# Optimization experiments

Hardware: AMD Instinct MI355X
Metric: run time of the kernel (lower is better)

Reference implementation:

```python
import jax, jax.numpy as jnp
import numpy as np


def setup_inputs() -> dict:
    key = jax.random.key(0)
    ks = jax.random.split(key, 9)
    B = 1024
    s = 0.05
    return {
        "x": jax.random.normal(ks[0], (B, 1024), dtype=jnp.float32),
        "u1": jax.random.normal(ks[1], (8, 8, 16), dtype=jnp.float32) * s,
        "u2": jax.random.normal(ks[2], (8, 8, 16), dtype=jnp.float32) * s,
        "u3": jax.random.normal(ks[3], (16, 16, 16), dtype=jnp.float32) * s,
        "b2": jax.random.normal(ks[4], (16, 16, 16), dtype=jnp.float32) * s,
        "b1_core": jax.random.normal(ks[5], (16, 16), dtype=jnp.float32) * s,
        "bias1": jax.random.normal(ks[6], (8, 8, 16), dtype=jnp.float32) * s,
        "fc2_w": jax.random.normal(ks[7], (10, 1024), dtype=jnp.float32) * s,
        "fc2_b": jax.random.normal(ks[8], (10,), dtype=jnp.float32) * s,
    }


def reference(x, u1, u2, u3, b2, b1_core, bias1, fc2_w, fc2_b):
    batch = x.shape[0]
    t = x.reshape(batch, 8, 8, 16)                       # z a b c
    t = jnp.einsum('zabc,ade->zbcde', t, u1)             # (z,8,16,8,16)
    t = jnp.einsum('zabcd,def->zabcef', t, b2)           # (z,8,16,8,16,16)
    t = jnp.einsum('zabcde,afd->zbcef', t, u2)           # (z,16,8,16,8)
    t = jnp.einsum('zabcd,ce->zabde', t, b1_core)        # (z,16,8,8,16)
    t = jnp.einsum('zabcd,aed->zbce', t, u3)             # (z,8,8,16)
    t = t + bias1
    h = jax.nn.relu(t.reshape(batch, 1024))
    return h @ fc2_w.T + fc2_b
```

## Files before the change

### kernel.cpp

```cpp
#include <hip/hip_runtime.h>


using s16x8 = __attribute__((ext_vector_type(8))) short;
using f32x4 = __attribute__((ext_vector_type(4))) float;

__device__ inline short f2bf(float f) {
    unsigned u = __builtin_bit_cast(unsigned, f);
    u += 0x7fffu + ((u >> 16) & 1u);
    return (short)(u >> 16);
}

__global__ __launch_bounds__(256) void k_prep(
    const float* __restrict__ x, const float* __restrict__ u1,
    const float* __restrict__ u2, const float* __restrict__ u3,
    const float* __restrict__ b2, const float* __restrict__ b1c,
    short* __restrict__ Wb, short* __restrict__ Xb) {
    const int blk = blockIdx.x;
    const int tid = threadIdx.x;

    if (blk >= 256) {
        const int base = (blk - 256) * 4096 + tid * 16;
#pragma unroll
        for (int h = 0; h < 2; ++h) {
            float4 f0 = *(const float4*)&x[base + h * 8];
            float4 f1 = *(const float4*)&x[base + h * 8 + 4];
            s16x8 v;
            v[0] = f2bf(f0.x); v[1] = f2bf(f0.y);
            v[2] = f2bf(f0.z); v[3] = f2bf(f0.w);
            v[4] = f2bf(f1.x); v[5] = f2bf(f1.y);
            v[6] = f2bf(f1.z); v[7] = f2bf(f1.w);
            *(s16x8*)&Xb[base + h * 8] = v;
        }
        return;
    }

    __shared__ float b1s[256];
    __shared__ float u1s[128];
    __shared__ float u2s[64 * 17];
    __shared__ float u3s[4096];
    __shared__ float C2t[256 * 17];
    __shared__ float T1s[2048];
    __shared__ float T2s[64 * 17];
    const int d = blk >> 5;
    const int r = (blk >> 2) & 7;
    const int t0 = (blk & 3) * 4;

    b1s[tid] = b1c[tid];
    {
        float4* dst = (float4*)u3s;
        const float4* src = (const float4*)u3;
#pragma unroll
        for (int q = 0; q < 4; ++q) dst[tid + 256 * q] = src[tid + 256 * q];
    }
    if (tid < 64) {
        const float4* src = (const float4*)&u2[tid * 16];
#pragma unroll
        for (int q = 0; q < 4; ++q) {
            float4 v = src[q];
            u2s[tid * 17 + q * 4 + 0] = v.x;
            u2s[tid * 17 + q * 4 + 1] = v.y;
            u2s[tid * 17 + q * 4 + 2] = v.z;
            u2s[tid * 17 + q * 4 + 3] = v.w;
        }
    }
    if (tid < 8) {
#pragma unroll
        for (int e = 0; e < 16; ++e)
            u1s[tid * 16 + e] = u1[(tid * 8 + d) * 16 + e];
    }
    float b2r[16];
    {
        const float4* src = (const float4*)&b2[tid * 16];
#pragma unroll
        for (int q = 0; q < 4; ++q) {
            float4 v = src[q];
            b2r[q * 4 + 0] = v.x; b2r[q * 4 + 1] = v.y;
            b2r[q * 4 + 2] = v.z; b2r[q * 4 + 3] = v.w;
        }
    }
    __syncthreads();

    {
        float accs[16] = {};
#pragma unroll
        for (int q = 0; q < 16; ++q) {
            const float bq = b2r[q];
#pragma unroll
            for (int s = 0; s < 16; ++s) accs[s] += bq * b1s[q * 16 + s];
        }
#pragma unroll
        for (int s = 0; s < 16; ++s) C2t[tid * 17 + s] = accs[s];
    }
    __syncthreads();

    {
        const int p = tid >> 4, s = tid & 15;
#pragma unroll
        for (int a = 0; a < 8; ++a) {
            float acc = 0.f;
#pragma unroll
            for (int e = 0; e < 16; ++e)
                acc += u1s[a * 16 + e] * C2t[(e * 16 + p) * 17 + s];
            T1s[a * 256 + tid] = acc;
        }
    }
    __syncthreads();

#pragma unroll
    for (int j = 0; j < 4; ++j) {
        int idx = tid + 256 * j;
        int ab = idx >> 4, s = idx & 15;
        int a = ab >> 3, b = ab & 7;
        float acc = 0.f;
#pragma unroll
        for (int p = 0; p < 16; ++p)
            acc += T1s[a * 256 + p * 16 + s] * u2s[(b * 8 + r) * 17 + p];
        T2s[ab * 17 + s] = acc;
    }
    __syncthreads();

    {
        const int j = tid >> 6;
        const int t = t0 + j;
        const int col0 = (tid & 63) * 16;
        const int ab = col0 >> 4;
        const float* t2p = &T2s[ab * 17];
        short* wrow = &Wb[(blk * 4 + j) * 1024 + col0];
        s16x8 v0, v1;
#pragma unroll
        for (int c = 0; c < 16; ++c) {
            const float* u3p = &u3s[c * 256 + t * 16];
            float acc = 0.f;
#pragma unroll
            for (int s = 0; s < 16; ++s) acc += t2p[s] * u3p[s];
            short bf = f2bf(acc);
            if (c < 8) v0[c] = bf; else v1[c - 8] = bf;
        }
        *(s16x8*)(wrow) = v0;
        *(s16x8*)(wrow + 8) = v1;
    }
}

#define LDK 136

__global__ __launch_bounds__(256) void k_gemm(
    const short* __restrict__ Xb, const short* __restrict__ Wb,
    float* __restrict__ PH) {
    __shared__ short As[64][LDK];
    __shared__ short Bs[64][LDK];
    const int tid = threadIdx.x;
    const int lane = tid & 63;
    const int w = tid >> 6, wr = w >> 1, wc = w & 1;
    const int o0 = blockIdx.x * 64, z0 = blockIdx.y * 64, kz = blockIdx.z;
    const int srow = tid >> 2;
    const int sc = (tid & 3) * 16;

    const short* xp = &Xb[(z0 + srow) * 1024 + kz * 256 + sc];
    const short* wp = &Wb[(o0 + srow) * 1024 + kz * 256 + sc];

    f32x4 acc[2][2] = {};
    s16x8 ax[4], bx[4];

#pragma unroll
    for (int h = 0; h < 2; ++h)
#pragma unroll
        for (int q = 0; q < 2; ++q) {
            ax[h * 2 + q] = *(const s16x8*)(xp + h * 64 + q * 8);
            bx[h * 2 + q] = *(const s16x8*)(wp + h * 64 + q * 8);
        }

#pragma unroll
    for (int it = 0; it < 2; ++it) {
#pragma unroll
        for (int h = 0; h < 2; ++h)
#pragma unroll
            for (int q = 0; q < 2; ++q) {
                *(s16x8*)&As[srow][sc + h * 64 + q * 8] = ax[h * 2 + q];
                *(s16x8*)&Bs[srow][sc + h * 64 + q * 8] = bx[h * 2 + q];
            }
        __syncthreads();
        if (it == 0) {
#pragma unroll
            for (int h = 0; h < 2; ++h)
#pragma unroll
                for (int q = 0; q < 2; ++q) {
                    ax[h * 2 + q] = *(const s16x8*)(xp + 128 + h * 64 + q * 8);
                    bx[h * 2 + q] = *(const s16x8*)(wp + 128 + h * 64 + q * 8);
                }
        }
#pragma unroll
        for (int ks = 0; ks < 4; ++ks) {
            const int kb = ks * 32 + (lane >> 4) * 8;
            s16x8 a0 = *(const s16x8*)&As[wr * 32 + (lane & 15)][kb];
            s16x8 a1 = *(const s16x8*)&As[wr * 32 + 16 + (lane & 15)][kb];
            s16x8 b0 = *(const s16x8*)&Bs[wc * 32 + (lane & 15)][kb];
            s16x8 b1 = *(const s16x8*)&Bs[wc * 32 + 16 + (lane & 15)][kb];
            acc[0][0] = __builtin_amdgcn_mfma_f32_16x16x32_bf16(a0, b0, acc[0][0], 0, 0, 0);
            acc[0][1] = __builtin_amdgcn_mfma_f32_16x16x32_bf16(a0, b1, acc[0][1], 0, 0, 0);
            acc[1][0] = __builtin_amdgcn_mfma_f32_16x16x32_bf16(a1, b0, acc[1][0], 0, 0, 0);
            acc[1][1] = __builtin_amdgcn_mfma_f32_16x16x32_bf16(a1, b1, acc[1][1], 0, 0, 0);
        }
        __syncthreads();
    }

    float* ph = &PH[(unsigned)kz * 1048576u];
#pragma unroll
    for (int m = 0; m < 2; ++m)
#pragma unroll
        for (int n = 0; n < 2; ++n) {
            const int row = z0 + wr * 32 + m * 16 + (lane >> 4) * 4;
            const int col = o0 + wc * 32 + n * 16 + (lane & 15);
#pragma unroll
            for (int j = 0; j < 4; ++j)
                ph[(row + j) * 1024 + col] = acc[m][n][j];
        }
}

__global__ __launch_bounds__(256) void k_out(
    const float* __restrict__ PH, const float* __restrict__ bias1,
    const float* __restrict__ W2, const float* __restrict__ fc2b,
    float* __restrict__ out) {
    __shared__ float W2s[10][1024];
    const int tid = threadIdx.x;
#pragma unroll
    for (int i = 0; i < 10; ++i) {
        const int idx = tid + 256 * i;
        ((float4*)W2s)[idx] = ((const float4*)W2)[idx];
    }
    __syncthreads();

    const int wid = tid >> 6, lane = tid & 63;
    const int z = blockIdx.x * 4 + wid;
    float part[10];
#pragma unroll
    for (int j = 0; j < 10; ++j) part[j] = 0.f;
#pragma unroll
    for (int i = 0; i < 16; ++i) {
        const int col = lane + 64 * i;
        float h = PH[z * 1024 + col] + PH[1048576 + z * 1024 + col]
                + PH[2097152 + z * 1024 + col] + PH[3145728 + z * 1024 + col];
        h = fmaxf(h + bias1[col], 0.f);
#pragma unroll
        for (int j = 0; j < 10; ++j) part[j] += h * W2s[j][col];
    }
#pragma unroll
    for (int j = 0; j < 10; ++j) {
#pragma unroll
        for (int off = 32; off > 0; off >>= 1) part[j] += __shfl_xor(part[j], off);
    }
    if (lane == 0) {
#pragma unroll
        for (int j = 0; j < 10; ++j) out[z * 10 + j] = part[j] + fc2b[j];
    }
}

extern "C" void kernel_launch(void* const* d_in, const int* in_sizes, int n_in,
                              void* d_out, int out_size, void* d_ws, size_t ws_size,
                              hipStream_t stream) {
    const float* x     = (const float*)d_in[0];
    const float* u1    = (const float*)d_in[1];
    const float* u2    = (const float*)d_in[2];
    const float* u3    = (const float*)d_in[3];
    const float* b2    = (const float*)d_in[4];
    const float* b1c   = (const float*)d_in[5];
    const float* bias1 = (const float*)d_in[6];
    const float* fc2w  = (const float*)d_in[7];
    const float* fc2b  = (const float*)d_in[8];
    float* out = (float*)d_out;

    short* Wb = (short*)d_ws;
    short* Xb = (short*)((char*)d_ws + 2u * 1024u * 1024u);
    float* PH = (float*)((char*)d_ws + 4u * 1024u * 1024u);

    k_prep<<<512, 256, 0, stream>>>(x, u1, u2, u3, b2, b1c, Wb, Xb);
    k_gemm<<<dim3(16, 16, 4), 256, 0, stream>>>(Xb, Wb, PH);
    k_out<<<256, 256, 0, stream>>>(PH, bias1, fc2w, fc2b, out);
}
```

Baseline: 29.03 us.

## Drop LDS staging in GEMM and load MFMA fragments directly from global

The split-K GEMM no longer stages A and B tiles in shared memory with barriers. Each of 8 waves loads its bf16 MFMA fragments straight from global memory and computes a 16x32 output slice over the full 256-long K chunk. This removes LDS writes, reads and syncs and doubles the waves per block. In exchange, A and B data is fetched redundantly across waves and relies on cache hits.

Result: slower. 44.17 us (+52.1%).

```diff
diff --git a/kernel.cpp b/kernel.cpp
--- a/kernel.cpp
+++ b/kernel.cpp
@@ -141,79 +141,41 @@
     }
 }
 
-#define LDK 136
-
-__global__ __launch_bounds__(256) void k_gemm(
+__global__ __launch_bounds__(512) void k_gemm(
     const short* __restrict__ Xb, const short* __restrict__ Wb,
     float* __restrict__ PH) {
-    __shared__ short As[64][LDK];
-    __shared__ short Bs[64][LDK];
     const int tid = threadIdx.x;
     const int lane = tid & 63;
-    const int w = tid >> 6, wr = w >> 1, wc = w & 1;
+    const int wid = tid >> 6;
+    const int band = wid >> 1;
+    const int half = wid & 1;
     const int o0 = blockIdx.x * 64, z0 = blockIdx.y * 64, kz = blockIdx.z;
-    const int srow = tid >> 2;
-    const int sc = (tid & 3) * 16;
-
-    const short* xp = &Xb[(z0 + srow) * 1024 + kz * 256 + sc];
-    const short* wp = &Wb[(o0 + srow) * 1024 + kz * 256 + sc];
-
-    f32x4 acc[2][2] = {};
-    s16x8 ax[4], bx[4];
-
-#pragma unroll
-    for (int h = 0; h < 2; ++h)
-#pragma unroll
-        for (int q = 0; q < 2; ++q) {
-            ax[h * 2 + q] = *(const s16x8*)(xp + h * 64 + q * 8);
-            bx[h * 2 + q] = *(const s16x8*)(wp + h * 64 + q * 8);
-        }
-
-#pragma unroll
-    for (int it = 0; it < 2; ++it) {
-#pragma unroll
-        for (int h = 0; h < 2; ++h)
-#pragma unroll
-            for (int q = 0; q < 2; ++q) {
-                *(s16x8*)&As[srow][sc + h * 64 + q * 8] = ax[h * 2 + q];
-                *(s16x8*)&Bs[srow][sc + h * 64 + q * 8] = bx[h * 2 + q];
-            }
-        __syncthreads();
-        if (it == 0) {
-#pragma unroll
-            for (int h = 0; h < 2; ++h)
-#pragma unroll
-                for (int q = 0; q < 2; ++q) {
-                    ax[h * 2 + q] = *(const s16x8*)(xp + 128 + h * 64 + q * 8);
-                    bx[h * 2 + q] = *(const s16x8*)(wp + 128 + h * 64 + q * 8);
-                }
-        }
-#pragma unroll
-        for (int ks = 0; ks < 4; ++ks) {
-            const int kb = ks * 32 + (lane >> 4) * 8;
-            s16x8 a0 = *(const s16x8*)&As[wr * 32 + (lane & 15)][kb];
-            s16x8 a1 = *(const s16x8*)&As[wr * 32 + 16 + (lane & 15)][kb];
-            s16x8 b0 = *(const s16x8*)&Bs[wc * 32 + (lane & 15)][kb];
-            s16x8 b1 = *(const s16x8*)&Bs[wc * 32 + 16 + (lane & 15)][kb];
-            acc[0][0] = __builtin_amdgcn_mfma_f32_16x16x32_bf16(a0, b0, acc[0][0], 0, 0, 0);
-            acc[0][1] = __builtin_amdgcn_mfma_f32_16x16x32_bf16(a0, b1, acc[0][1], 0, 0, 0);
-            acc[1][0] = __builtin_amdgcn_mfma_f32_16x16x32_bf16(a1, b0, acc[1][0], 0, 0, 0);
-            acc[1][1] = __builtin_amdgcn_mfma_f32_16x16x32_bf16(a1, b1, acc[1][1], 0, 0, 0);
-        }
-        __syncthreads();
+    const int lr = lane & 15, lk = lane >> 4;
+
+    const short* ap  = &Xb[(z0 + band * 16 + lr) * 1024 + kz * 256 + lk * 8];
+    const short* b0p = &Wb[(o0 + half * 32 + lr) * 1024 + kz * 256 + lk * 8];
+    const short* b1p = b0p + 16 * 1024;
+
+    f32x4 acc[2] = {};
+#pragma unroll
+    for (int k8 = 0; k8 < 8; ++k8) {
+        const int off = k8 * 32;
+        s16x8 av = *(const s16x8*)(ap + off);
+        s16x8 b0 = *(const s16x8*)(b0p + off);
+        s16x8 b1 = *(const s16x8*)(b1p + off);
+        acc[0] = __builtin_amdgcn_mfma_f32_16x16x32_bf16(av, b0, acc[0], 0, 0, 0);
+        acc[1] = __builtin_amdgcn_mfma_f32_16x16x32_bf16(av, b1, acc[1], 0, 0, 0);
     }
 
     float* ph = &PH[(unsigned)kz * 1048576u];
 #pragma unroll
-    for (int m = 0; m < 2; ++m)
-#pragma unroll
-        for (int n = 0; n < 2; ++n) {
-            const int row = z0 + wr * 32 + m * 16 + (lane >> 4) * 4;
-            const int col = o0 + wc * 32 + n * 16 + (lane & 15);
-#pragma unroll
-            for (int j = 0; j < 4; ++j)
-                ph[(row + j) * 1024 + col] = acc[m][n][j];
-        }
+    for (int n = 0; n < 2; ++n) {
+        const int col = o0 + half * 32 + n * 16 + lr;
+        const int row = z0 + band * 16 + lk * 4;
+#pragma unroll
+        for (int j = 0; j < 4; ++j)
+            ph[(row + j) * 1024 + col] = acc[n][j];
+    }
 }
 
 __global__ __launch_bounds__(256) void k_out(
@@ -273,6 +235,6 @@
     float* PH = (float*)((char*)d_ws + 4u * 1024u * 1024u);
 
     k_prep<<<512, 256, 0, stream>>>(x, u1, u2, u3, b2, b1c, Wb, Xb);
-    k_gemm<<<dim3(16, 16, 4), 256, 0, stream>>>(Xb, Wb, PH);
+    k_gemm<<<dim3(16, 16, 4), 512, 0, stream>>>(Xb, Wb, PH);
     k_out<<<256, 256, 0, stream>>>(PH, bias1, fc2w, fc2b, out);
 }
```
